# Kernel optimization log

Hardware: AMD Instinct MI355X
Metric: run time of the kernel (lower is better)

The kernel has to match this reference:

```python
import jax, jax.numpy as jnp
import numpy as np
import math

HEAD_DIM = 64

def setup_inputs() -> dict:
    key = jax.random.key(0)
    k1, k2, k3, k4 = jax.random.split(key, 4)
    B, T, E, H = 4096, 128, 256, HEAD_DIM
    x = jax.random.normal(k1, (B, T, E), dtype=jnp.float32)
    # torch nn.Linear init scale ~ U(-1/sqrt(E), 1/sqrt(E)); use scaled normal for simplicity
    s = 1.0 / math.sqrt(E)
    Wq = jax.random.normal(k2, (E, H), dtype=jnp.float32) * s
    Wk = jax.random.normal(k3, (E, H), dtype=jnp.float32) * s
    Wv = jax.random.normal(k4, (E, H), dtype=jnp.float32) * s
    return {"x": x, "Wq": Wq, "Wk": Wk, "Wv": Wv}

def reference(x, Wq, Wk, Wv):
    # x: [B, T, E]; Wq/Wk/Wv: [E, H]
    T = x.shape[1]
    H = Wq.shape[1]
    Q = jnp.einsum('bte,eh->bth', x, Wq)
    K = jnp.einsum('bte,eh->bth', x, Wk)
    V = jnp.einsum('bte,eh->bth', x, Wv)
    scores = jnp.einsum('bqh,bkh->bqk', Q, K) / jnp.sqrt(jnp.float32(H))  # [B,T,T]
    causal = jnp.tril(jnp.ones((T, T), dtype=bool))
    scores = jnp.where(causal, scores, -jnp.inf)
    weights = jax.nn.softmax(scores, axis=-1)
    # dropout omitted (eval mode / deterministic reference)
    out = jnp.einsum('bqk,bkh->bqh', weights, V)  # [B,T,H]
    return out
```

## Files before the change

### kernel.cpp

```cpp
#include <hip/hip_runtime.h>

#define NB 4096
#define TT 128
#define EE 256
#define HH 64

typedef __attribute__((ext_vector_type(8))) short bf16x8;
typedef __attribute__((ext_vector_type(4))) float f32x4;

#define QK_STRIDE 72
#define P_STRIDE  136
#define VT_STRIDE 136

__device__ __forceinline__ unsigned short f2bf(float f) {
  union { float f; unsigned u; } c; c.f = f;
  return (unsigned short)((c.u + 0x7fffu + ((c.u >> 16) & 1u)) >> 16);
}

__device__ __forceinline__ bf16x8 cvt8(f32x4 a, f32x4 b) {
  bf16x8 r;
  r[0] = (short)f2bf(a[0]); r[1] = (short)f2bf(a[1]);
  r[2] = (short)f2bf(a[2]); r[3] = (short)f2bf(a[3]);
  r[4] = (short)f2bf(b[0]); r[5] = (short)f2bf(b[1]);
  r[6] = (short)f2bf(b[2]); r[7] = (short)f2bf(b[3]);
  return r;
}

__global__ void prep_w(const float* __restrict__ wq, const float* __restrict__ wk,
                       const float* __restrict__ wv, unsigned short* __restrict__ wt) {
  int n = blockIdx.x;
  int e = threadIdx.x;
  const float* w = (n < 64) ? wq : (n < 128) ? wk : wv;
  wt[n * EE + e] = f2bf(w[e * HH + (n & 63)]);
}

__global__ __launch_bounds__(256, 2)
void attn_fused(const float* __restrict__ x, const unsigned short* __restrict__ wt,
                float* __restrict__ out) {
  __shared__ __align__(16) unsigned short sQK[2 * TT * QK_STRIDE];
  __shared__ __align__(16) unsigned short sVT[HH * VT_STRIDE];
  unsigned short* qbuf = sQK;
  unsigned short* kbuf = sQK + TT * QK_STRIDE;
  unsigned short* pbuf = sQK;

  const int b    = blockIdx.x;
  const int tid  = threadIdx.x;
  const int w    = tid >> 6;
  const int lane = tid & 63;
  const int quad = lane >> 4;
  const int l16  = lane & 15;
  const int m0   = 32 * w;

  const float* __restrict__ xb = x + (size_t)b * TT * EE;

  f32x4 acc[12][2];
#pragma unroll
  for (int nt = 0; nt < 12; ++nt)
#pragma unroll
    for (int mt = 0; mt < 2; ++mt)
      acc[nt][mt] = (f32x4){0.f, 0.f, 0.f, 0.f};

  for (int kc = 0; kc < 8; ++kc) {
    bf16x8 afr[2];
#pragma unroll
    for (int mt = 0; mt < 2; ++mt) {
      const float* src = xb + (m0 + 16 * mt + l16) * EE + kc * 32 + quad * 8;
      f32x4 f0 = *(const f32x4*)src;
      f32x4 f1 = *(const f32x4*)(src + 4);
      afr[mt] = cvt8(f0, f1);
    }
#pragma unroll
    for (int nt = 0; nt < 12; ++nt) {
      bf16x8 bfr = *(const bf16x8*)(wt + (nt * 16 + l16) * EE + kc * 32 + quad * 8);
      acc[nt][0] = __builtin_amdgcn_mfma_f32_16x16x32_bf16(afr[0], bfr, acc[nt][0], 0, 0, 0);
      acc[nt][1] = __builtin_amdgcn_mfma_f32_16x16x32_bf16(afr[1], bfr, acc[nt][1], 0, 0, 0);
    }
  }

#pragma unroll
  for (int nt = 0; nt < 12; ++nt) {
    int cg = nt * 16 + l16;
#pragma unroll
    for (int mt = 0; mt < 2; ++mt) {
      int rbase = m0 + 16 * mt + 4 * quad;
#pragma unroll
      for (int r = 0; r < 4; ++r) {
        unsigned short bv = f2bf(acc[nt][mt][r]);
        int row = rbase + r;
        if (nt < 4)      qbuf[row * QK_STRIDE + cg] = bv;
        else if (nt < 8) kbuf[row * QK_STRIDE + (cg - 64)] = bv;
        else             sVT[(cg - 128) * VT_STRIDE + row] = bv;
      }
    }
  }
  __syncthreads();

  const int ntS = 2 * w + 2;
  f32x4 sacc[8][2];
#pragma unroll
  for (int nt = 0; nt < 8; ++nt)
#pragma unroll
    for (int mt = 0; mt < 2; ++mt)
      sacc[nt][mt] = (f32x4){0.f, 0.f, 0.f, 0.f};

#pragma unroll
  for (int kk = 0; kk < 2; ++kk) {
    bf16x8 aq[2];
    aq[0] = *(const bf16x8*)(qbuf + (m0 + l16) * QK_STRIDE + kk * 32 + quad * 8);
    aq[1] = *(const bf16x8*)(qbuf + (m0 + 16 + l16) * QK_STRIDE + kk * 32 + quad * 8);
#pragma unroll
    for (int nt = 0; nt < 8; ++nt) {
      if (nt < ntS) {
        bf16x8 bk = *(const bf16x8*)(kbuf + (nt * 16 + l16) * QK_STRIDE + kk * 32 + quad * 8);
        sacc[nt][0] = __builtin_amdgcn_mfma_f32_16x16x32_bf16(aq[0], bk, sacc[nt][0], 0, 0, 0);
        sacc[nt][1] = __builtin_amdgcn_mfma_f32_16x16x32_bf16(aq[1], bk, sacc[nt][1], 0, 0, 0);
      }
    }
  }
  __syncthreads();

  const float scale = 0.125f;
#pragma unroll
  for (int mt = 0; mt < 2; ++mt) {
#pragma unroll
    for (int r = 0; r < 4; ++r) {
      int row = m0 + 16 * mt + 4 * quad + r;
      float mx = -3.0e38f;
#pragma unroll
      for (int nt = 0; nt < 8; ++nt) {
        if (nt < ntS) {
          int c = nt * 16 + l16;
          float s = (c <= row) ? sacc[nt][mt][r] * scale : -3.0e38f;
          sacc[nt][mt][r] = s;
          mx = fmaxf(mx, s);
        }
      }
#pragma unroll
      for (int off = 1; off < 16; off <<= 1) mx = fmaxf(mx, __shfl_xor(mx, off, 64));
      float sum = 0.f;
#pragma unroll
      for (int nt = 0; nt < 8; ++nt) {
        if (nt < ntS) {
          float e = __expf(sacc[nt][mt][r] - mx);
          sacc[nt][mt][r] = e;
          sum += e;
        }
      }
#pragma unroll
      for (int off = 1; off < 16; off <<= 1) sum += __shfl_xor(sum, off, 64);
      float inv = 1.0f / sum;
#pragma unroll
      for (int nt = 0; nt < 8; ++nt) {
        if (nt < ntS)
          pbuf[row * P_STRIDE + nt * 16 + l16] = f2bf(sacc[nt][mt][r] * inv);
      }
    }
  }

  f32x4 oacc[4][2];
#pragma unroll
  for (int nt = 0; nt < 4; ++nt)
#pragma unroll
    for (int mt = 0; mt < 2; ++mt)
      oacc[nt][mt] = (f32x4){0.f, 0.f, 0.f, 0.f};

  for (int ks = 0; ks <= w; ++ks) {
    bf16x8 ap[2];
    ap[0] = *(const bf16x8*)(pbuf + (m0 + l16) * P_STRIDE + ks * 32 + quad * 8);
    ap[1] = *(const bf16x8*)(pbuf + (m0 + 16 + l16) * P_STRIDE + ks * 32 + quad * 8);
#pragma unroll
    for (int nt = 0; nt < 4; ++nt) {
      bf16x8 bv = *(const bf16x8*)(sVT + (nt * 16 + l16) * VT_STRIDE + ks * 32 + quad * 8);
      oacc[nt][0] = __builtin_amdgcn_mfma_f32_16x16x32_bf16(ap[0], bv, oacc[nt][0], 0, 0, 0);
      oacc[nt][1] = __builtin_amdgcn_mfma_f32_16x16x32_bf16(ap[1], bv, oacc[nt][1], 0, 0, 0);
    }
  }

  float* __restrict__ ob = out + (size_t)b * TT * HH;
#pragma unroll
  for (int mt = 0; mt < 2; ++mt) {
#pragma unroll
    for (int r = 0; r < 4; ++r) {
      int row = m0 + 16 * mt + 4 * quad + r;
#pragma unroll
      for (int nt = 0; nt < 4; ++nt)
        ob[row * HH + nt * 16 + l16] = oacc[nt][mt][r];
    }
  }
}

extern "C" void kernel_launch(void* const* d_in, const int* in_sizes, int n_in,
                              void* d_out, int out_size, void* d_ws, size_t ws_size,
                              hipStream_t stream) {
  const float* x  = (const float*)d_in[0];
  const float* wq = (const float*)d_in[1];
  const float* wk = (const float*)d_in[2];
  const float* wv = (const float*)d_in[3];
  unsigned short* wt = (unsigned short*)d_ws;
  float* outp = (float*)d_out;

  prep_w<<<dim3(192), dim3(256), 0, stream>>>(wq, wk, wv, wt);
  attn_fused<<<dim3(NB), dim3(256), 0, stream>>>(x, wt, outp);
}
```

Before: 901.0 us.

## Swizzle unpadded LDS layouts, split projection into three passes, raise occupancy

Replaces the padded shared-memory strides with XOR-swizzled unpadded layouts for Q, K, P and V^T. This shrinks LDS from about 54KB to 48KB and targets bank conflicts. The QKV projection now preloads all of x as bf16 fragments and runs three 64-column passes, so only 8 accumulators are live instead of 24. Launch bounds move from 2 to 3 blocks per CU to allow more blocks resident. V^T is written with packed 4-element stores. The risks are register spills from holding 16 x fragments, and the extra index arithmetic.

New measurement: 980.3 us. 1.09x slower.

```diff
diff --git a/kernel.cpp b/kernel.cpp
--- a/kernel.cpp
+++ b/kernel.cpp
@@ -7,10 +7,7 @@
 
 typedef __attribute__((ext_vector_type(8))) short bf16x8;
 typedef __attribute__((ext_vector_type(4))) float f32x4;
-
-#define QK_STRIDE 72
-#define P_STRIDE  136
-#define VT_STRIDE 136
+typedef __attribute__((ext_vector_type(4))) unsigned short u16x4;
 
 __device__ __forceinline__ unsigned short f2bf(float f) {
   union { float f; unsigned u; } c; c.f = f;
@@ -26,6 +23,16 @@
   return r;
 }
 
+__device__ __forceinline__ int qk_idx(int t, int h) {
+  return t * 64 + ((((h >> 3) ^ t) & 7) << 3) + (h & 7);
+}
+__device__ __forceinline__ int p_idx(int t, int c) {
+  return t * 128 + ((((c >> 3) ^ t) & 15) << 3) + (c & 7);
+}
+__device__ __forceinline__ int vt_idx(int h, int t) {
+  return h * 128 + ((((t >> 3) ^ h) & 15) << 3) + (t & 7);
+}
+
 __global__ void prep_w(const float* __restrict__ wq, const float* __restrict__ wk,
                        const float* __restrict__ wv, unsigned short* __restrict__ wt) {
   int n = blockIdx.x;
@@ -34,14 +41,14 @@
   wt[n * EE + e] = f2bf(w[e * HH + (n & 63)]);
 }
 
-__global__ __launch_bounds__(256, 2)
+__global__ __launch_bounds__(256, 3)
 void attn_fused(const float* __restrict__ x, const unsigned short* __restrict__ wt,
                 float* __restrict__ out) {
-  __shared__ __align__(16) unsigned short sQK[2 * TT * QK_STRIDE];
-  __shared__ __align__(16) unsigned short sVT[HH * VT_STRIDE];
-  unsigned short* qbuf = sQK;
-  unsigned short* kbuf = sQK + TT * QK_STRIDE;
-  unsigned short* pbuf = sQK;
+  __shared__ __align__(16) unsigned short sbuf[24576];
+  unsigned short* qbuf = sbuf;
+  unsigned short* kbuf = sbuf + 8192;
+  unsigned short* vbuf = sbuf + 16384;
+  unsigned short* pbuf = sbuf;
 
   const int b    = blockIdx.x;
   const int tid  = threadIdx.x;
@@ -53,43 +60,58 @@
 
   const float* __restrict__ xb = x + (size_t)b * TT * EE;
 
-  f32x4 acc[12][2];
-#pragma unroll
-  for (int nt = 0; nt < 12; ++nt)
-#pragma unroll
-    for (int mt = 0; mt < 2; ++mt)
-      acc[nt][mt] = (f32x4){0.f, 0.f, 0.f, 0.f};
-
+  bf16x8 axf[8][2];
+#pragma unroll
   for (int kc = 0; kc < 8; ++kc) {
-    bf16x8 afr[2];
 #pragma unroll
     for (int mt = 0; mt < 2; ++mt) {
       const float* src = xb + (m0 + 16 * mt + l16) * EE + kc * 32 + quad * 8;
       f32x4 f0 = *(const f32x4*)src;
       f32x4 f1 = *(const f32x4*)(src + 4);
-      afr[mt] = cvt8(f0, f1);
-    }
-#pragma unroll
-    for (int nt = 0; nt < 12; ++nt) {
-      bf16x8 bfr = *(const bf16x8*)(wt + (nt * 16 + l16) * EE + kc * 32 + quad * 8);
-      acc[nt][0] = __builtin_amdgcn_mfma_f32_16x16x32_bf16(afr[0], bfr, acc[nt][0], 0, 0, 0);
-      acc[nt][1] = __builtin_amdgcn_mfma_f32_16x16x32_bf16(afr[1], bfr, acc[nt][1], 0, 0, 0);
-    }
-  }
-
-#pragma unroll
-  for (int nt = 0; nt < 12; ++nt) {
-    int cg = nt * 16 + l16;
-#pragma unroll
-    for (int mt = 0; mt < 2; ++mt) {
-      int rbase = m0 + 16 * mt + 4 * quad;
-#pragma unroll
-      for (int r = 0; r < 4; ++r) {
-        unsigned short bv = f2bf(acc[nt][mt][r]);
-        int row = rbase + r;
-        if (nt < 4)      qbuf[row * QK_STRIDE + cg] = bv;
-        else if (nt < 8) kbuf[row * QK_STRIDE + (cg - 64)] = bv;
-        else             sVT[(cg - 128) * VT_STRIDE + row] = bv;
+      axf[kc][mt] = cvt8(f0, f1);
+    }
+  }
+
+#pragma unroll
+  for (int pass = 0; pass < 3; ++pass) {
+    f32x4 acc[4][2];
+#pragma unroll
+    for (int j = 0; j < 4; ++j)
+#pragma unroll
+      for (int mt = 0; mt < 2; ++mt)
+        acc[j][mt] = (f32x4){0.f, 0.f, 0.f, 0.f};
+
+#pragma unroll
+    for (int kc = 0; kc < 8; ++kc) {
+#pragma unroll
+      for (int j = 0; j < 4; ++j) {
+        int nt = pass * 4 + j;
+        bf16x8 bfr = *(const bf16x8*)(wt + (nt * 16 + l16) * EE + kc * 32 + quad * 8);
+        acc[j][0] = __builtin_amdgcn_mfma_f32_16x16x32_bf16(axf[kc][0], bfr, acc[j][0], 0, 0, 0);
+        acc[j][1] = __builtin_amdgcn_mfma_f32_16x16x32_bf16(axf[kc][1], bfr, acc[j][1], 0, 0, 0);
+      }
+    }
+
+#pragma unroll
+    for (int j = 0; j < 4; ++j) {
+      int col = j * 16 + l16;
+#pragma unroll
+      for (int mt = 0; mt < 2; ++mt) {
+        int rbase = m0 + 16 * mt + 4 * quad;
+        if (pass == 0) {
+#pragma unroll
+          for (int r = 0; r < 4; ++r)
+            qbuf[qk_idx(rbase + r, col)] = f2bf(acc[j][mt][r]);
+        } else if (pass == 1) {
+#pragma unroll
+          for (int r = 0; r < 4; ++r)
+            kbuf[qk_idx(rbase + r, col)] = f2bf(acc[j][mt][r]);
+        } else {
+          u16x4 pk;
+          pk[0] = f2bf(acc[j][mt][0]); pk[1] = f2bf(acc[j][mt][1]);
+          pk[2] = f2bf(acc[j][mt][2]); pk[3] = f2bf(acc[j][mt][3]);
+          *(u16x4*)(vbuf + vt_idx(col, rbase)) = pk;
+        }
       }
     }
   }
@@ -106,12 +128,12 @@
 #pragma unroll
   for (int kk = 0; kk < 2; ++kk) {
     bf16x8 aq[2];
-    aq[0] = *(const bf16x8*)(qbuf + (m0 + l16) * QK_STRIDE + kk * 32 + quad * 8);
-    aq[1] = *(const bf16x8*)(qbuf + (m0 + 16 + l16) * QK_STRIDE + kk * 32 + quad * 8);
+    aq[0] = *(const bf16x8*)(qbuf + qk_idx(m0 + l16, kk * 32 + quad * 8));
+    aq[1] = *(const bf16x8*)(qbuf + qk_idx(m0 + 16 + l16, kk * 32 + quad * 8));
 #pragma unroll
     for (int nt = 0; nt < 8; ++nt) {
       if (nt < ntS) {
-        bf16x8 bk = *(const bf16x8*)(kbuf + (nt * 16 + l16) * QK_STRIDE + kk * 32 + quad * 8);
+        bf16x8 bk = *(const bf16x8*)(kbuf + qk_idx(nt * 16 + l16, kk * 32 + quad * 8));
         sacc[nt][0] = __builtin_amdgcn_mfma_f32_16x16x32_bf16(aq[0], bk, sacc[nt][0], 0, 0, 0);
         sacc[nt][1] = __builtin_amdgcn_mfma_f32_16x16x32_bf16(aq[1], bk, sacc[nt][1], 0, 0, 0);
       }
@@ -152,7 +174,7 @@
 #pragma unroll
       for (int nt = 0; nt < 8; ++nt) {
         if (nt < ntS)
-          pbuf[row * P_STRIDE + nt * 16 + l16] = f2bf(sacc[nt][mt][r] * inv);
+          pbuf[p_idx(row, nt * 16 + l16)] = f2bf(sacc[nt][mt][r] * inv);
       }
     }
   }
@@ -166,11 +188,11 @@
 
   for (int ks = 0; ks <= w; ++ks) {
     bf16x8 ap[2];
-    ap[0] = *(const bf16x8*)(pbuf + (m0 + l16) * P_STRIDE + ks * 32 + quad * 8);
-    ap[1] = *(const bf16x8*)(pbuf + (m0 + 16 + l16) * P_STRIDE + ks * 32 + quad * 8);
+    ap[0] = *(const bf16x8*)(pbuf + p_idx(m0 + l16, ks * 32 + quad * 8));
+    ap[1] = *(const bf16x8*)(pbuf + p_idx(m0 + 16 + l16, ks * 32 + quad * 8));
 #pragma unroll
     for (int nt = 0; nt < 4; ++nt) {
-      bf16x8 bv = *(const bf16x8*)(sVT + (nt * 16 + l16) * VT_STRIDE + ks * 32 + quad * 8);
+      bf16x8 bv = *(const bf16x8*)(vbuf + vt_idx(nt * 16 + l16, ks * 32 + quad * 8));
       oacc[nt][0] = __builtin_amdgcn_mfma_f32_16x16x32_bf16(ap[0], bv, oacc[nt][0], 0, 0, 0);
       oacc[nt][1] = __builtin_amdgcn_mfma_f32_16x16x32_bf16(ap[1], bv, oacc[nt][1], 0, 0, 0);
     }
```
